# Optimization experiments

Measured on AMD Instinct MI355X. Metric: run time of the kernel, lower is better.

The kernel has to match this reference:

```python
import jax, jax.numpy as jnp
import numpy as np

H = 16  # attention heads


def setup_inputs() -> dict:
    key = jax.random.key(0)
    k0, k1, k2 = jax.random.split(key, 3)
    B, T, C = 2, 2048, 1024
    x = jax.random.normal(k0, (B, T, C), dtype=jnp.float32)
    W_attn = jax.random.normal(k1, (3 * C, C), dtype=jnp.float32) * 0.02
    W_proj = jax.random.normal(k2, (C, C), dtype=jnp.float32) * 0.02
    b_proj = jnp.zeros((C,), dtype=jnp.float32)
    return {"x": x, "W_attn": W_attn, "W_proj": W_proj, "b_proj": b_proj}


def reference(x, W_attn, W_proj, b_proj):
    # Eval-mode (dropout = identity), rotational_embeddings=False, flash=False path.
    B, T, C = x.shape
    d = C // H
    qkv = jnp.einsum('btc,fc->btf', x, W_attn)          # [B,T,3C] fused QKV proj
    q, k, v = jnp.split(qkv, 3, axis=-1)
    # [B,T,C] -> [B,H,T,d]
    q = q.reshape(B, T, H, d).transpose(0, 2, 1, 3)
    k = k.reshape(B, T, H, d).transpose(0, 2, 1, 3)
    v = v.reshape(B, T, H, d).transpose(0, 2, 1, 3)
    scale = 1.0 / np.sqrt(d).astype(np.float32)
    att = jnp.einsum('bhqd,bhkd->bhqk', q, k) * scale    # full TxT scores (no mask)
    att = jax.nn.softmax(att, axis=-1)
    y = jnp.einsum('bhqk,bhkd->bhqd', att, v)            # [B,H,T,d]
    y = y.transpose(0, 2, 1, 3).reshape(B, T, C)
    return jnp.einsum('btc,oc->bto', y, W_proj) + b_proj
```

## Files before the change

### kernel.cpp

```cpp
#include <hip/hip_runtime.h>
#include <hip/hip_bf16.h>
#include <stdint.h>

typedef __attribute__((ext_vector_type(8))) short bf16x8;
typedef __attribute__((ext_vector_type(4))) float f32x4;
typedef __attribute__((ext_vector_type(4))) unsigned u32x4;

#define MFMA16(A,B,C) __builtin_amdgcn_mfma_f32_16x16x32_bf16(A,B,C,0,0,0)


__device__ inline void gld_lds16(const __hip_bfloat16* g, __hip_bfloat16* l) {
  __builtin_amdgcn_global_load_lds(
      (const __attribute__((address_space(1))) void*)g,
      (__attribute__((address_space(3))) void*)l, 16, 0, 0);
}

__device__ inline unsigned pkbf(float a, float b) {
  __hip_bfloat162 t = __float22bfloat162_rn(float2{a, b});
  return *(unsigned*)&t;
}

__device__ inline void quad_mix(unsigned &a, unsigned &b) {
#if __has_builtin(__builtin_amdgcn_permlane32_swap) && __has_builtin(__builtin_amdgcn_permlane16_swap)
  auto r1 = __builtin_amdgcn_permlane32_swap(a, b, false, false);
  auto r2 = __builtin_amdgcn_permlane16_swap(r1[0], r1[1], false, false);
  a = r2[0];
  b = r2[1];
#else
  int lane = (int)(threadIdx.x & 63);
  int g = lane >> 4;
  int lm = lane & 15;
  int slo = (((g << 1) & 3) << 4) | lm;
  int shi = ((((g << 1) | 1) & 3) << 4) | lm;
  unsigned t0 = (unsigned)__shfl((int)a, slo, 64);
  unsigned t1 = (unsigned)__shfl((int)b, slo, 64);
  unsigned t2 = (unsigned)__shfl((int)a, shi, 64);
  unsigned t3 = (unsigned)__shfl((int)b, shi, 64);
  bool hi = g >= 2;
  unsigned na = hi ? t1 : t0;
  unsigned nb = hi ? t3 : t2;
  a = na;
  b = nb;
#endif
}

__global__ __launch_bounds__(256)
void cvt_bf16(const float* __restrict__ s0, __hip_bfloat16* __restrict__ d0, int n0,
              const float* __restrict__ s1, __hip_bfloat16* __restrict__ d1, int n1,
              const float* __restrict__ s2, __hip_bfloat16* __restrict__ d2, int n2)
{
  const float* s; __hip_bfloat16* d; int n;
  if      (blockIdx.y == 0) { s = s0; d = d0; n = n0; }
  else if (blockIdx.y == 1) { s = s1; d = d1; n = n1; }
  else                      { s = s2; d = d2; n = n2; }
  int idx = (blockIdx.x * 256 + threadIdx.x) * 8;
  if (idx >= n) return;
  float4 u0 = *(const float4*)(s + idx);
  float4 u1 = *(const float4*)(s + idx + 4);
  __hip_bfloat16 t[8];
  t[0] = __float2bfloat16(u0.x); t[1] = __float2bfloat16(u0.y);
  t[2] = __float2bfloat16(u0.z); t[3] = __float2bfloat16(u0.w);
  t[4] = __float2bfloat16(u1.x); t[5] = __float2bfloat16(u1.y);
  t[6] = __float2bfloat16(u1.z); t[7] = __float2bfloat16(u1.w);
  *(int4*)(d + idx) = *(const int4*)t;
}

template<int BM, int BN, typename TC, bool VT, bool FUSE>
__global__ __launch_bounds__(256)
void gemm_bt(const __hip_bfloat16* __restrict__ A,
             const __hip_bfloat16* __restrict__ B,
             TC* __restrict__ C,
             const float* __restrict__ bias,
             __hip_bfloat16* __restrict__ vtg,
             const float* __restrict__ pl,
             int M, int N, int K)
{
  constexpr int MI  = BM / 32;
  constexpr int NJ  = BN / 32;
  constexpr int ACH = BM * 8;
  constexpr int NP  = (BM + BN) * 8 / 256;

  __shared__ __align__(16) __hip_bfloat16 smem[(BM + BN) * 64];
  __hip_bfloat16* As = smem;
  __hip_bfloat16* Bs = smem + BM * 64;

  const int tid  = threadIdx.x;
  const int lane = tid & 63;
  const int w    = tid >> 6;
  const int lm   = lane & 15;
  const int g    = lane >> 4;
  const int sx   = lm & 7;

  int bxs = blockIdx.x, bys = blockIdx.y;
  {
    const int nwg = gridDim.x * gridDim.y;
    if ((nwg & 7) == 0) {
      int lid = bys * gridDim.x + bxs;
      int nl = (lid & 7) * (nwg >> 3) + (lid >> 3);
      bxs = nl % gridDim.x;
      bys = nl / gridDim.x;
    }
  }
  const int bm = bys * BM;
  const int bn = bxs * BN;
  const int rm = (w >> 1) * (BM / 2);
  const int cn = (w & 1) * (BN / 2);

  const f32x4 fzero = {0.0f, 0.0f, 0.0f, 0.0f};
  f32x4 acc[MI][NJ];
  for (int i = 0; i < MI; i++)
    for (int j = 0; j < NJ; j++)
      acc[i][j] = fzero;

  for (int k0 = 0; k0 < K; k0 += 64) {
    __syncthreads();
#pragma unroll
    for (int p = 0; p < NP; p++) {
      int c = tid + p * 256;
      if (c < ACH) {
        int row = c >> 3, sl = c & 7, gc = sl ^ (row & 7);
        if constexpr (FUSE) {
          int grow = bm + row;
          int col  = k0 + gc * 8;
          int hh   = col >> 6;
          float li = pl[grow * 16 + hh] + pl[(size_t)M * 16 + grow * 16 + hh];
          float rinv = 1.0f / li;
          int4 ra = *(const int4*)&A[(size_t)grow * K + col];
          int4 rb = *(const int4*)&A[(size_t)M * K + (size_t)grow * K + col];
          const __hip_bfloat16* pa = (const __hip_bfloat16*)&ra;
          const __hip_bfloat16* pb = (const __hip_bfloat16*)&rb;
          __hip_bfloat16 tt[8];
#pragma unroll
          for (int jj = 0; jj < 8; jj++)
            tt[jj] = __float2bfloat16(
                (__bfloat162float(pa[jj]) + __bfloat162float(pb[jj])) * rinv);
          *(int4*)&As[c * 8] = *(const int4*)tt;
        } else {
          gld_lds16(&A[(size_t)(bm + row) * K + k0 + gc * 8], &As[c * 8]);
        }
      } else {
        int cb = c - ACH;
        int row = cb >> 3, sl = cb & 7, gc = sl ^ (row & 7);
        gld_lds16(&B[(size_t)(bn + row) * K + k0 + gc * 8], &Bs[cb * 8]);
      }
    }
    __syncthreads();

#pragma unroll
    for (int e = 0; e < 2; e++) {
      bf16x8 af[MI], bfr[NJ];
#pragma unroll
      for (int i = 0; i < MI; i++)
        af[i] = *(const bf16x8*)
            &As[(rm + 16 * i + lm) * 64 + ((4 * e + g) ^ sx) * 8];
#pragma unroll
      for (int j = 0; j < NJ; j++)
        bfr[j] = *(const bf16x8*)
            &Bs[(cn + 16 * j + lm) * 64 + ((4 * e + g) ^ sx) * 8];
#pragma unroll
      for (int i = 0; i < MI; i++)
#pragma unroll
        for (int j = 0; j < NJ; j++)
          acc[i][j] = MFMA16(af[i], bfr[j], acc[i][j]);
    }
  }

  if constexpr (VT) {
    if (vtg != nullptr && bn >= 2048) {
      __syncthreads();
      __hip_bfloat16* scr = smem + w * (32 * 72);
      const int vh = (bn + cn - 2048) >> 6;
      const int m0 = bm + rm;
      const int bb = m0 >> 11, t0 = m0 & 2047;
      const int cc = lane & 7, rl = lane >> 3;
#pragma unroll
      for (int p = 0; p < 2; p++) {
#pragma unroll
        for (int jj = 0; jj < 2; jj++) {
          int j = 2 * p + jj;
#pragma unroll
          for (int i = 0; i < MI; i++) {
            __hip_bfloat16 t4[4];
#pragma unroll
            for (int r = 0; r < 4; r++) t4[r] = __float2bfloat16(acc[i][j][r]);
            *(int2*)&scr[(16 * jj + lm) * 72 + 16 * i + 4 * g] =
                *(const int2*)t4;
          }
        }
        asm volatile("s_waitcnt lgkmcnt(0)" ::: "memory");
        __builtin_amdgcn_sched_barrier(0);
#pragma unroll
        for (int it = 0; it < 4; it++) {
          int lr = it * 8 + rl;
          int dd = 32 * p + lr;
          int4 vrow = *(const int4*)&scr[lr * 72 + cc * 8];
          *(int4*)&vtg[((size_t)(bb * 16 + vh) * 64 + dd) * 2048 + t0 + cc * 8] =
              vrow;
        }
        asm volatile("s_waitcnt lgkmcnt(0)" ::: "memory");
        __builtin_amdgcn_sched_barrier(0);
      }
      return;
    }
  }

  const float qs = (VT && vtg != nullptr && bn < 1024)
                       ? (0.125f * 1.4426950408889634f) : 1.0f;

  if constexpr (sizeof(TC) == 2 && MI == 4) {
    __syncthreads();
    __hip_bfloat16* scr = smem + w * (32 * 72);
    const int cc = lane & 7, rl = lane >> 3;
#pragma unroll
    for (int p = 0; p < 2; p++) {
#pragma unroll
      for (int ii = 0; ii < 2; ii++) {
        int i = 2 * p + ii;
#pragma unroll
        for (int j = 0; j < NJ; j++) {
          float bv = bias ? bias[bn + cn + 16 * j + lm] : 0.0f;
#pragma unroll
          for (int r = 0; r < 4; r++) {
            float v = acc[i][j][r] * qs + bv;
            scr[(16 * ii + 4 * g + r) * 72 + 16 * j + lm] = __float2bfloat16(v);
          }
        }
      }
      asm volatile("s_waitcnt lgkmcnt(0)" ::: "memory");
      __builtin_amdgcn_sched_barrier(0);
#pragma unroll
      for (int it = 0; it < 4; it++) {
        int lr = it * 8 + rl;
        int rowm = bm + rm + 32 * p + lr;
        int4 vrow = *(const int4*)&scr[lr * 72 + cc * 8];
        *(int4*)&C[(size_t)rowm * N + bn + cn + cc * 8] = vrow;
      }
      asm volatile("s_waitcnt lgkmcnt(0)" ::: "memory");
      __builtin_amdgcn_sched_barrier(0);
    }
    return;
  }

#pragma unroll
  for (int j = 0; j < NJ; j++) {
    int coln = bn + cn + 16 * j + lm;
    float bv = bias ? bias[coln] : 0.0f;
#pragma unroll
    for (int i = 0; i < MI; i++) {
#pragma unroll
      for (int r = 0; r < 4; r++) {
        int rowm = bm + rm + 16 * i + 4 * g + r;
        float v = acc[i][j][r] * qs + bv;
        if constexpr (sizeof(TC) == 2)
          C[(size_t)rowm * N + coln] = __float2bfloat16(v);
        else
          C[(size_t)rowm * N + coln] = v;
      }
    }
  }
}

__global__ __launch_bounds__(256)
void mha(const __hip_bfloat16* __restrict__ qkv,
         const __hip_bfloat16* __restrict__ vtg,
         __hip_bfloat16* __restrict__ yout,
         __hip_bfloat16* __restrict__ po,
         float* __restrict__ pl,
         int nsteps)
{
  const int T = 2048, F = 3072, Cc = 1024;
  const int bh = blockIdx.x;
  const int b  = bh >> 4, h = bh & 15;
  const int qb0 = blockIdx.y * 128;
  const int z   = blockIdx.z;
  const int kvb = z * 64 * nsteps;

  const int tid  = threadIdx.x;
  const int lane = tid & 63;
  const int w    = tid >> 6;
  const int lm   = lane & 15;
  const int g    = lane >> 4;

  __shared__ __align__(16) __hip_bfloat16 Ks[2][64 * 64];
  __shared__ __align__(16) __hip_bfloat16 Vs[2][64 * 64];

  const size_t rowbase = (size_t)b * T * F;
  const int hoff = h * 64;
  const __hip_bfloat16* Kbase = qkv + rowbase + 1024 + hoff;
  const __hip_bfloat16* Vtb   = vtg + (size_t)(b * 16 + h) * 64 * 2048;

  const int qw = qb0 + 32 * w;
  bf16x8 aq[2][2];
#pragma unroll
  for (int mt = 0; mt < 2; mt++)
#pragma unroll
    for (int e = 0; e < 2; e++)
      aq[mt][e] = *(const bf16x8*)
          &qkv[rowbase + (size_t)(qw + 16 * mt + lm) * F + hoff + 32 * e + 8 * g];

  const f32x4 fzero = {0.0f, 0.0f, 0.0f, 0.0f};
  const short one_bf = (short)0x3f80;
  const bf16x8 vone = {one_bf, one_bf, one_bf, one_bf,
                       one_bf, one_bf, one_bf, one_bf};
  f32x4 yacc[2][4];
  f32x4 yl[2];
#pragma unroll
  for (int mt = 0; mt < 2; mt++) {
    yl[mt] = fzero;
#pragma unroll
    for (int c = 0; c < 4; c++) yacc[mt][c] = fzero;
  }

  const int sx = lm & 7;

  auto stage = [&](int tt, int bb) {
    const int kvn = kvb + tt * 64;
#pragma unroll
    for (int p = 0; p < 2; p++) {
      int c = tid + p * 256;
      int row = c >> 3, sl = c & 7, gc = sl ^ (row & 7);
      gld_lds16(Kbase + (size_t)(kvn + row) * F + gc * 8, &Ks[bb][c * 8]);
    }
#pragma unroll
    for (int p = 0; p < 2; p++) {
      int c = tid + p * 256;
      int row = c >> 3, sl = c & 7, gc = sl ^ (row & 7);
      gld_lds16(Vtb + (size_t)row * 2048 + kvn + gc * 8, &Vs[bb][c * 8]);
    }
  };

  stage(0, 0);

  for (int t = 0; t < nsteps; t++) {
    const int buf = t & 1;
    __syncthreads();
    if (t + 1 < nsteps) stage(t + 1, buf ^ 1);

    const __hip_bfloat16* Kb = Ks[buf];
    const __hip_bfloat16* Vb = Vs[buf];

    f32x4 st[2][4];
    __builtin_amdgcn_s_setprio(1);
#pragma unroll
    for (int c2 = 0; c2 < 4; c2++) {
      bf16x8 k0 = *(const bf16x8*)&Kb[(16 * c2 + lm) * 64 + ((0 + g) ^ sx) * 8];
      bf16x8 k1 = *(const bf16x8*)&Kb[(16 * c2 + lm) * 64 + ((4 + g) ^ sx) * 8];
      st[0][c2] = MFMA16(k0, aq[0][0], fzero);
      st[0][c2] = MFMA16(k1, aq[0][1], st[0][c2]);
      st[1][c2] = MFMA16(k0, aq[1][0], fzero);
      st[1][c2] = MFMA16(k1, aq[1][1], st[1][c2]);
    }
    __builtin_amdgcn_s_setprio(0);

    bf16x8 ap[2][2];
#pragma unroll
    for (int mt = 0; mt < 2; mt++) {
#pragma unroll
      for (int hf = 0; hf < 2; hf++) {
        unsigned pkv[2][2];
#pragma unroll
        for (int cc = 0; cc < 2; cc++) {
          const f32x4 &s4 = st[mt][2 * hf + cc];
#pragma unroll
          for (int u = 0; u < 2; u++) {
            float p0 = __builtin_amdgcn_exp2f(s4[2 * u]);
            float p1 = __builtin_amdgcn_exp2f(s4[2 * u + 1]);
            pkv[cc][u] = pkbf(p0, p1);
          }
        }
        unsigned f0 = pkv[0][0], f2 = pkv[1][0];
        quad_mix(f0, f2);
        unsigned f1 = pkv[0][1], f3 = pkv[1][1];
        quad_mix(f1, f3);
        u32x4 fv = {f0, f1, f2, f3};
        ap[mt][hf] = __builtin_bit_cast(bf16x8, fv);
      }
    }

    __builtin_amdgcn_s_setprio(1);
#pragma unroll
    for (int c = 0; c < 4; c++) {
#pragma unroll
      for (int hf = 0; hf < 2; hf++) {
        bf16x8 bv = *(const bf16x8*)
            &Vb[(16 * c + lm) * 64 + (((hf << 2) | g) ^ sx) * 8];
        yacc[0][c] = MFMA16(ap[0][hf], bv, yacc[0][c]);
        yacc[1][c] = MFMA16(ap[1][hf], bv, yacc[1][c]);
      }
    }
#pragma unroll
    for (int mt = 0; mt < 2; mt++) {
      yl[mt] = MFMA16(ap[mt][0], vone, yl[mt]);
      yl[mt] = MFMA16(ap[mt][1], vone, yl[mt]);
    }
    __builtin_amdgcn_s_setprio(0);
  }

#pragma unroll
  for (int mt = 0; mt < 2; mt++) {
    if (yout != nullptr) {
      float rv[4];
#pragma unroll
      for (int r = 0; r < 4; r++)
        rv[r] = 1.0f / yl[mt][r];
#pragma unroll
      for (int c = 0; c < 4; c++)
#pragma unroll
        for (int r = 0; r < 4; r++) {
          int qrow = qw + 16 * mt + 4 * g + r;
          yout[(size_t)(b * T + qrow) * Cc + hoff + 16 * c + lm] =
              __float2bfloat16(yacc[mt][c][r] * rv[r]);
        }
    } else {
      __hip_bfloat16* pz = po + (size_t)z * 4096 * 1024;
      float* plz = pl + (size_t)z * 4096 * 16;
#pragma unroll
      for (int c = 0; c < 4; c++)
#pragma unroll
        for (int r = 0; r < 4; r++) {
          int qrow = qw + 16 * mt + 4 * g + r;
          pz[(size_t)(b * T + qrow) * Cc + hoff + 16 * c + lm] =
              __float2bfloat16(yacc[mt][c][r]);
        }
      if (lm == 0) {
#pragma unroll
        for (int r = 0; r < 4; r++)
          plz[(b * T + qw + 16 * mt + 4 * g + r) * 16 + h] = yl[mt][r];
      }
    }
  }
}

extern "C" void kernel_launch(void* const* d_in, const int* in_sizes, int n_in,
                              void* d_out, int out_size, void* d_ws, size_t ws_size,
                              hipStream_t stream)
{
  const float* x  = (const float*)d_in[0];
  const float* Wa = (const float*)d_in[1];
  const float* Wp = (const float*)d_in[2];
  const float* bp = (const float*)d_in[3];
  float* out = (float*)d_out;

  const int BT = 4096, C = 1024, F3 = 3072;
  char* ws = (char*)d_ws;
  __hip_bfloat16* qkv  = (__hip_bfloat16*)ws;
  __hip_bfloat16* vtg  = (__hip_bfloat16*)(ws + 25165824);
  __hip_bfloat16* xbf  = (__hip_bfloat16*)(ws + 33554432);
  __hip_bfloat16* yb   = xbf;
  __hip_bfloat16* Wabf = (__hip_bfloat16*)(ws + 41943040);
  __hip_bfloat16* Wpbf = (__hip_bfloat16*)(ws + 48234496);
  __hip_bfloat16* Opar = (__hip_bfloat16*)(ws + 50331648);
  float*          lpar = (float*)(ws + 67108864);
  const size_t need_split = 67633152;

  cvt_bf16<<<dim3(2048, 3), 256, 0, stream>>>(
      x, xbf, BT * C, Wa, Wabf, F3 * C, Wp, Wpbf, C * C);
  gemm_bt<128, 128, __hip_bfloat16, true, false>
      <<<dim3(F3 / 128, BT / 128), 256, 0, stream>>>(xbf, Wabf, qkv, nullptr, vtg,
                                                     nullptr, BT, F3, C);
  if (ws_size >= need_split) {
    mha<<<dim3(32, 16, 2), 256, 0, stream>>>(qkv, vtg, nullptr, Opar, lpar, 16);
    gemm_bt<64, 128, float, false, true>
        <<<dim3(C / 128, BT / 64), 256, 0, stream>>>(Opar, Wpbf, out, bp,
                                                     nullptr, lpar, BT, C, C);
  } else {
    mha<<<dim3(32, 16, 1), 256, 0, stream>>>(qkv, vtg, yb, nullptr, nullptr, 32);
    gemm_bt<64, 128, float, false, false>
        <<<dim3(C / 128, BT / 64), 256, 0, stream>>>(yb, Wpbf, out, bp,
                                                     nullptr, nullptr, BT, C, C);
  }
}
```

Baseline: 190.0 us.

## Add dedicated 256x256 QKV projection GEMM with double-buffered LDS prefetch

Replaces the generic 128x128 QKV projection GEMM with a specialised 512-thread kernel using 256x256 tiles, double-buffered async global-to-LDS loads interleaved with MFMA sub-blocks, an XCD-aware block remap and wave priority hints. The epilogue writes scaled Q, K and transposed V as before. It aims to raise operand reuse and overlap loads with compute. The cost is only 192 workgroups, fewer than the CUs, and a large LDS footprint limiting occupancy. The old VT and bf16 epilogue paths in the generic GEMM are removed as now unused.

```diff
diff --git a/kernel.cpp b/kernel.cpp
--- a/kernel.cpp
+++ b/kernel.cpp
@@ -65,6 +65,189 @@
   *(int4*)(d + idx) = *(const int4*)t;
 }
 
+__global__ __launch_bounds__(512)
+void gemm1_256(const __hip_bfloat16* __restrict__ A,
+               const __hip_bfloat16* __restrict__ B,
+               __hip_bfloat16* __restrict__ C,
+               __hip_bfloat16* __restrict__ vtg)
+{
+  const int K = 1024, N = 3072, NKT = 16;
+  __shared__ __align__(16) __hip_bfloat16 smem[65536];
+  __hip_bfloat16* As0 = smem;
+  __hip_bfloat16* Bs0 = smem + 32768;
+
+  const int tid  = threadIdx.x;
+  const int lane = tid & 63;
+  const int w    = tid >> 6;
+  const int lm   = lane & 15;
+  const int g    = lane >> 4;
+  const int sx   = lm & 7;
+  const int wr   = w >> 2;
+  const int wc   = w & 3;
+
+  int bxs = blockIdx.x, bys = blockIdx.y;
+  {
+    const int nwg = gridDim.x * gridDim.y;
+    if ((nwg & 7) == 0) {
+      int lid = bys * gridDim.x + bxs;
+      int nl = (lid & 7) * (nwg >> 3) + (lid >> 3);
+      bxs = nl % gridDim.x;
+      bys = nl / gridDim.x;
+    }
+  }
+  const int bm = bys * 256;
+  const int bn = bxs * 256;
+
+  const f32x4 fzero = {0.0f, 0.0f, 0.0f, 0.0f};
+  f32x4 acc[8][4];
+#pragma unroll
+  for (int i = 0; i < 8; i++)
+#pragma unroll
+    for (int j = 0; j < 4; j++) acc[i][j] = fzero;
+
+  auto stageA = [&](int kt, int h) {
+    __hip_bfloat16* dst = As0 + (kt & 1) * 16384;
+    const int kb = kt * 64;
+#pragma unroll
+    for (int p = 0; p < 2; p++) {
+      int c = tid + p * 512;
+      int row = c >> 3, sl = c & 7, gc = sl ^ (row & 7);
+      int rowg = h * 128 + row;
+      gld_lds16(&A[(size_t)(bm + rowg) * K + kb + gc * 8],
+                &dst[rowg * 64 + sl * 8]);
+    }
+  };
+  auto stageB = [&](int kt, int h) {
+    __hip_bfloat16* dst = Bs0 + (kt & 1) * 16384;
+    const int kb = kt * 64;
+#pragma unroll
+    for (int p = 0; p < 2; p++) {
+      int c = tid + p * 512;
+      int row = c >> 3, sl = c & 7, gc = sl ^ (row & 7);
+      int rowg = h * 128 + row;
+      gld_lds16(&B[(size_t)(bn + rowg) * K + kb + gc * 8],
+                &dst[rowg * 64 + sl * 8]);
+    }
+  };
+
+  stageA(0, 0); stageA(0, 1); stageB(0, 0); stageB(0, 1);
+
+  for (int kt = 0; kt < NKT; kt++) {
+    const int bq = kt & 1;
+    asm volatile("s_waitcnt vmcnt(0)" ::: "memory");
+    __builtin_amdgcn_s_barrier();
+    __builtin_amdgcn_sched_barrier(0);
+    const __hip_bfloat16* Ab = As0 + bq * 16384;
+    const __hip_bfloat16* Bb = Bs0 + bq * 16384;
+
+#pragma unroll
+    for (int qa = 0; qa < 2; qa++) {
+      bf16x8 af[4][2];
+#pragma unroll
+      for (int i2 = 0; i2 < 4; i2++)
+#pragma unroll
+        for (int kk = 0; kk < 2; kk++)
+          af[i2][kk] = *(const bf16x8*)
+              &Ab[(wr * 128 + qa * 64 + 16 * i2 + lm) * 64 +
+                  ((kk * 4 + g) ^ sx) * 8];
+#pragma unroll
+      for (int qb = 0; qb < 2; qb++) {
+        bf16x8 bfr[2][2];
+#pragma unroll
+        for (int j2 = 0; j2 < 2; j2++)
+#pragma unroll
+          for (int kk = 0; kk < 2; kk++)
+            bfr[j2][kk] = *(const bf16x8*)
+                &Bb[(wc * 64 + qb * 32 + 16 * j2 + lm) * 64 +
+                    ((kk * 4 + g) ^ sx) * 8];
+
+        if (kt + 1 < NKT) {
+          int q = qa * 2 + qb;
+          if      (q == 0) stageA(kt + 1, 0);
+          else if (q == 1) stageA(kt + 1, 1);
+          else if (q == 2) stageB(kt + 1, 0);
+          else             stageB(kt + 1, 1);
+        }
+        __builtin_amdgcn_s_barrier();
+        __builtin_amdgcn_s_setprio(1);
+#pragma unroll
+        for (int i2 = 0; i2 < 4; i2++)
+#pragma unroll
+          for (int j2 = 0; j2 < 2; j2++) {
+            acc[qa * 4 + i2][qb * 2 + j2] =
+                MFMA16(af[i2][0], bfr[j2][0], acc[qa * 4 + i2][qb * 2 + j2]);
+            acc[qa * 4 + i2][qb * 2 + j2] =
+                MFMA16(af[i2][1], bfr[j2][1], acc[qa * 4 + i2][qb * 2 + j2]);
+          }
+        __builtin_amdgcn_s_setprio(0);
+        __builtin_amdgcn_s_barrier();
+      }
+    }
+  }
+
+  __syncthreads();
+  __hip_bfloat16* scr = smem + w * 4608;
+  const int cc = lane & 7, rl = lane >> 3;
+
+  if (bn < 2048) {
+    const float qs = (bn < 1024) ? (0.125f * 1.4426950408889634f) : 1.0f;
+#pragma unroll
+    for (int pp = 0; pp < 2; pp++) {
+#pragma unroll
+      for (int ii = 0; ii < 4; ii++)
+#pragma unroll
+        for (int jj = 0; jj < 4; jj++)
+#pragma unroll
+          for (int r = 0; r < 4; r++)
+            scr[(16 * ii + 4 * g + r) * 72 + 16 * jj + lm] =
+                __float2bfloat16(acc[4 * pp + ii][jj][r] * qs);
+      asm volatile("s_waitcnt lgkmcnt(0)" ::: "memory");
+      __builtin_amdgcn_sched_barrier(0);
+#pragma unroll
+      for (int it = 0; it < 8; it++) {
+        int lr = it * 8 + rl;
+        int rowm = bm + wr * 128 + pp * 64 + lr;
+        int4 vrow = *(const int4*)&scr[lr * 72 + cc * 8];
+        *(int4*)&C[(size_t)rowm * N + bn + wc * 64 + cc * 8] = vrow;
+      }
+      asm volatile("s_waitcnt lgkmcnt(0)" ::: "memory");
+      __builtin_amdgcn_sched_barrier(0);
+    }
+    return;
+  }
+
+  {
+    const int vh = (bn + wc * 64 - 2048) >> 6;
+    const int m0 = bm + wr * 128;
+    const int bb = m0 >> 11, t0 = m0 & 2047;
+#pragma unroll
+    for (int pp = 0; pp < 2; pp++) {
+#pragma unroll
+      for (int ii = 0; ii < 4; ii++)
+#pragma unroll
+        for (int jj = 0; jj < 4; jj++) {
+          __hip_bfloat16 t4[4];
+#pragma unroll
+          for (int r = 0; r < 4; r++)
+            t4[r] = __float2bfloat16(acc[4 * pp + ii][jj][r]);
+          *(int2*)&scr[(16 * jj + lm) * 72 + 16 * ii + 4 * g] =
+              *(const int2*)t4;
+        }
+      asm volatile("s_waitcnt lgkmcnt(0)" ::: "memory");
+      __builtin_amdgcn_sched_barrier(0);
+#pragma unroll
+      for (int it = 0; it < 8; it++) {
+        int ddl = it * 8 + rl;
+        int4 vrow = *(const int4*)&scr[ddl * 72 + cc * 8];
+        *(int4*)&vtg[((size_t)(bb * 16 + vh) * 64 + ddl) * 2048 + t0 +
+                     pp * 64 + cc * 8] = vrow;
+      }
+      asm volatile("s_waitcnt lgkmcnt(0)" ::: "memory");
+      __builtin_amdgcn_sched_barrier(0);
+    }
+  }
+}
+
 template<int BM, int BN, typename TC, bool VT, bool FUSE>
 __global__ __launch_bounds__(256)
 void gemm_bt(const __hip_bfloat16* __restrict__ A,
@@ -165,82 +348,8 @@
     }
   }
 
-  if constexpr (VT) {
-    if (vtg != nullptr && bn >= 2048) {
-      __syncthreads();
-      __hip_bfloat16* scr = smem + w * (32 * 72);
-      const int vh = (bn + cn - 2048) >> 6;
-      const int m0 = bm + rm;
-      const int bb = m0 >> 11, t0 = m0 & 2047;
-      const int cc = lane & 7, rl = lane >> 3;
-#pragma unroll
-      for (int p = 0; p < 2; p++) {
-#pragma unroll
-        for (int jj = 0; jj < 2; jj++) {
-          int j = 2 * p + jj;
-#pragma unroll
-          for (int i = 0; i < MI; i++) {
-            __hip_bfloat16 t4[4];
-#pragma unroll
-            for (int r = 0; r < 4; r++) t4[r] = __float2bfloat16(acc[i][j][r]);
-            *(int2*)&scr[(16 * jj + lm) * 72 + 16 * i + 4 * g] =
-                *(const int2*)t4;
-          }
-        }
-        asm volatile("s_waitcnt lgkmcnt(0)" ::: "memory");
-        __builtin_amdgcn_sched_barrier(0);
-#pragma unroll
-        for (int it = 0; it < 4; it++) {
-          int lr = it * 8 + rl;
-          int dd = 32 * p + lr;
-          int4 vrow = *(const int4*)&scr[lr * 72 + cc * 8];
-          *(int4*)&vtg[((size_t)(bb * 16 + vh) * 64 + dd) * 2048 + t0 + cc * 8] =
-              vrow;
-        }
-        asm volatile("s_waitcnt lgkmcnt(0)" ::: "memory");
-        __builtin_amdgcn_sched_barrier(0);
-      }
-      return;
-    }
-  }
-
   const float qs = (VT && vtg != nullptr && bn < 1024)
                        ? (0.125f * 1.4426950408889634f) : 1.0f;
-
-  if constexpr (sizeof(TC) == 2 && MI == 4) {
-    __syncthreads();
-    __hip_bfloat16* scr = smem + w * (32 * 72);
-    const int cc = lane & 7, rl = lane >> 3;
-#pragma unroll
-    for (int p = 0; p < 2; p++) {
-#pragma unroll
-      for (int ii = 0; ii < 2; ii++) {
-        int i = 2 * p + ii;
-#pragma unroll
-        for (int j = 0; j < NJ; j++) {
-          float bv = bias ? bias[bn + cn + 16 * j + lm] : 0.0f;
-#pragma unroll
-          for (int r = 0; r < 4; r++) {
-            float v = acc[i][j][r] * qs + bv;
-            scr[(16 * ii + 4 * g + r) * 72 + 16 * j + lm] = __float2bfloat16(v);
-          }
-        }
-      }
-      asm volatile("s_waitcnt lgkmcnt(0)" ::: "memory");
-      __builtin_amdgcn_sched_barrier(0);
-#pragma unroll
-      for (int it = 0; it < 4; it++) {
-        int lr = it * 8 + rl;
-        int rowm = bm + rm + 32 * p + lr;
-        int4 vrow = *(const int4*)&scr[lr * 72 + cc * 8];
-        *(int4*)&C[(size_t)rowm * N + bn + cn + cc * 8] = vrow;
-      }
-      asm volatile("s_waitcnt lgkmcnt(0)" ::: "memory");
-      __builtin_amdgcn_sched_barrier(0);
-    }
-    return;
-  }
-
 #pragma unroll
   for (int j = 0; j < NJ; j++) {
     int coln = bn + cn + 16 * j + lm;
@@ -441,7 +550,7 @@
   const float* bp = (const float*)d_in[3];
   float* out = (float*)d_out;
 
-  const int BT = 4096, C = 1024, F3 = 3072;
+  const int BT = 4096, C = 1024;
   char* ws = (char*)d_ws;
   __hip_bfloat16* qkv  = (__hip_bfloat16*)ws;
   __hip_bfloat16* vtg  = (__hip_bfloat16*)(ws + 25165824);
@@ -454,10 +563,8 @@
   const size_t need_split = 67633152;
 
   cvt_bf16<<<dim3(2048, 3), 256, 0, stream>>>(
-      x, xbf, BT * C, Wa, Wabf, F3 * C, Wp, Wpbf, C * C);
-  gemm_bt<128, 128, __hip_bfloat16, true, false>
-      <<<dim3(F3 / 128, BT / 128), 256, 0, stream>>>(xbf, Wabf, qkv, nullptr, vtg,
-                                                     nullptr, BT, F3, C);
+      x, xbf, BT * C, Wa, Wabf, 3072 * C, Wp, Wpbf, C * C);
+  gemm1_256<<<dim3(12, 16), 512, 0, stream>>>(xbf, Wabf, qkv, vtg);
   if (ws_size >= need_split) {
     mha<<<dim3(32, 16, 2), 256, 0, stream>>>(qkv, vtg, nullptr, Opar, lpar, 16);
     gemm_bt<64, 128, float, false, true>
```

Result: slower. 196.8 us (+3.6%).
